# Kernel optimization log

Hardware: AMD Instinct MI355X
Metric: run time of the kernel (lower is better)

Reference implementation:

```python
import jax, jax.numpy as jnp
import numpy as np

B, T, IN = 256, 60, 520
GATE_IN = 8                      # 5 + 3, hard-coded in module
MOE_RAW = IN - GATE_IN           # 512
MOE_IN = MOE_RAW + GATE_IN * T   # 992
HID = MOE_RAW + (GATE_IN * T) // 2  # 752 (Python precedence: a + b*c//2)
OUT = 512
E = 8


def _uniform(key, shape, bound):
    return jax.random.uniform(key, shape, jnp.float32, -bound, bound)


def setup_inputs() -> dict:
    key = jax.random.key(0)
    ks = jax.random.split(key, 16)
    X = jax.random.normal(ks[0], (B, T, IN), jnp.float32)
    # GRU: 2 layers, hidden = E, gate order r,z,n (torch convention)
    gb = 1.0 / np.sqrt(E)
    Wih0 = _uniform(ks[1], (3 * E, GATE_IN), gb)
    Whh0 = _uniform(ks[2], (3 * E, E), gb)
    bih0 = _uniform(ks[3], (3 * E,), gb)
    bhh0 = _uniform(ks[4], (3 * E,), gb)
    Wih1 = _uniform(ks[5], (3 * E, E), gb)
    Whh1 = _uniform(ks[6], (3 * E, E), gb)
    bih1 = _uniform(ks[7], (3 * E,), gb)
    bhh1 = _uniform(ks[8], (3 * E,), gb)
    # Expert banks: glorot-style uniform as in init_params, zero biases
    def bank(k, i, o):
        wb = np.sqrt(6.0 / (i * o))
        return _uniform(k, (E, i, o), wb)
    w1 = bank(ks[9], MOE_IN, HID); b1 = jnp.zeros((E, HID), jnp.float32)
    w2 = bank(ks[10], HID, HID);   b2 = jnp.zeros((E, HID), jnp.float32)
    w3 = bank(ks[11], HID, OUT);   b3 = jnp.zeros((E, OUT), jnp.float32)
    return dict(X=X, Wih0=Wih0, Whh0=Whh0, bih0=bih0, bhh0=bhh0,
                Wih1=Wih1, Whh1=Whh1, bih1=bih1, bhh1=bhh1,
                w1=w1, b1=b1, w2=w2, b2=b2, w3=w3, b3=b3)


def _gru_layer(x, Wih, Whh, bih, bhh):
    # x: [B, T, in] -> outputs [B, T, H]
    H = Whh.shape[1]
    h0 = jnp.zeros((x.shape[0], H), x.dtype)

    def step(h, xt):
        gi = xt @ Wih.T + bih
        gh = h @ Whh.T + bhh
        ir, iz, i_n = jnp.split(gi, 3, axis=-1)
        hr, hz, h_n = jnp.split(gh, 3, axis=-1)
        r = jax.nn.sigmoid(ir + hr)
        z = jax.nn.sigmoid(iz + hz)
        n = jnp.tanh(i_n + r * h_n)
        h_new = (1.0 - z) * n + z * h
        return h_new, h_new

    _, ys = jax.lax.scan(step, h0, jnp.swapaxes(x, 0, 1))
    return jnp.swapaxes(ys, 0, 1)


def _blend_layer(x, coef, w, b):
    # per-sample weight synthesis + apply: same math as
    # sum(coef[...,None,None]*w[None],dim=1) then sum(x[...,None]*W,dim=1)+b
    Wb = jnp.einsum('be,eih->bih', coef, w)   # [B, in, out]
    bb = coef @ b                              # [B, out]
    return jnp.einsum('bi,bih->bh', x, Wb) + bb


def reference(X, Wih0, Whh0, bih0, bhh0, Wih1, Whh1, bih1, bhh1,
              w1, b1, w2, b2, w3, b3):
    Xg = X[:, :, MOE_RAW:]                                   # [B, T, 8]
    Xm = jnp.concatenate(
        [X[:, -1, :MOE_RAW], X[:, :, -GATE_IN:].reshape(X.shape[0], -1)], -1)
    # gating: 2-layer GRU, softmax on last step of layer 2
    h1 = _gru_layer(Xg, Wih0, Whh0, bih0, bhh0)
    h2 = _gru_layer(h1, Wih1, Whh1, bih1, bhh1)
    Omega = jax.nn.softmax(h2[:, -1, :], axis=-1)            # [B, E]
    # expert MLP with blended per-sample weights
    a = jax.nn.elu(_blend_layer(Xm, Omega, w1, b1))
    a = jax.nn.elu(_blend_layer(a, Omega, w2, b2))
    Y = _blend_layer(a, Omega, w3, b3)
    return Y
```

## Files before the change

kernel.cpp:

```cpp
#include <hip/hip_runtime.h>
#include <cstdint>
#include <cstddef>

typedef __attribute__((ext_vector_type(8))) short short8;
typedef __attribute__((ext_vector_type(8))) unsigned short ushort8;
typedef __attribute__((ext_vector_type(4))) float f32x4;

#define AS1Q const __attribute__((address_space(1)))
#define AS3Q __attribute__((address_space(3)))

constexpr int T_N = 60, IN_N = 520, MOE_RAW_N = 512, MOE_IN_N = 992;
constexpr int HID_N = 752, E_N = 8;
constexpr int K2_N = 6016;
constexpr int KA_N = 1024;
constexpr int SPLITK = 20;

static __device__ __forceinline__ unsigned short f2bf(float f) {
  unsigned int u = __float_as_uint(f);
  return (unsigned short)((u + 0x7fffu + ((u >> 16) & 1u)) >> 16);
}
static __device__ __forceinline__ float sigf(float x) {
  return __fdividef(1.f, 1.f + __expf(-x));
}
static __device__ __forceinline__ float tanh_fast(float x) {
  return 2.f * __fdividef(1.f, 1.f + __expf(-2.f * x)) - 1.f;
}

template<int R>
static __device__ __forceinline__ float rotf(float v) {
  return __int_as_float(__builtin_amdgcn_update_dpp(
      0, __float_as_int(v), 0x120 | R, 0xF, 0xF, true));
}
static __device__ __forceinline__ void rot8(float (&d)[8], float v) {
  d[0] = v;
  d[1] = rotf<1>(v); d[2] = rotf<2>(v); d[3] = rotf<3>(v);
  d[4] = rotf<4>(v); d[5] = rotf<5>(v); d[6] = rotf<6>(v); d[7] = rotf<7>(v);
}

__global__ __launch_bounds__(256)
void xm_prep(const float* __restrict__ X, unsigned short* __restrict__ XmBf)
{
  const int i = blockIdx.x * 256 + threadIdx.x;
  const int b = blockIdx.y;
  const float* Xb = X + (size_t)b * (T_N * IN_N);
  float v = 0.f;
  if (i < MOE_RAW_N) {
    v = Xb[(T_N - 1) * IN_N + i];
  } else if (i < MOE_IN_N) {
    const int q = i - MOE_RAW_N;
    v = Xb[(q >> 3) * IN_N + MOE_RAW_N + (q & 7)];
  }
  XmBf[(size_t)b * KA_N + (i ^ ((b & 7) << 3))] = f2bf(v);
}

__global__ __launch_bounds__(256, 1)
void fused_gru_gemm1(const float* __restrict__ X,
                     const float* __restrict__ Wih0, const float* __restrict__ Whh0,
                     const float* __restrict__ bih0, const float* __restrict__ bhh0,
                     const float* __restrict__ Wih1, const float* __restrict__ Whh1,
                     const float* __restrict__ bih1, const float* __restrict__ bhh1,
                     const unsigned short* __restrict__ XmBf,
                     const float* __restrict__ w1,
                     float* __restrict__ Y1, float* __restrict__ Omega)
{
  __shared__ union SM {
    struct { unsigned short Al[2][256][64]; unsigned short Bl[2][64][64]; } g;
    float xl[T_N][256];
  } sm;

  const int tid  = threadIdx.x;
  const int lane = tid & 63;
  const int wave = tid >> 6;

  if (blockIdx.x < 16) {
    const int j = tid & 7;
    const int b = blockIdx.x * 16 + (tid >> 4);

    const float* xsrc = X + (size_t)b * (T_N * IN_N) + MOE_RAW_N + j;
#pragma unroll
    for (int t = 0; t < T_N; ++t) {
      __builtin_amdgcn_global_load_lds((AS1Q unsigned int*)(xsrc + t * IN_N),
                                       (AS3Q unsigned int*)&sm.xl[t][wave * 64], 4, 0, 0);
    }

    const int got = __builtin_amdgcn_update_dpp(0, j, 0x121, 0xF, 0xF, true);
    const bool plus = (got == ((j + 1) & 7));

    float wi0r[8], wi0z[8], wi0n[8], wh0r[8], wh0z[8], wh0n[8];
    float wi1r[8], wi1z[8], wi1n[8], wh1r[8], wh1z[8], wh1n[8];
#pragma unroll
    for (int r = 0; r < 8; ++r) {
      const int i = plus ? ((j + r) & 7) : ((j - r) & 7);
      wi0r[r] = Wih0[j * 8 + i]; wi0z[r] = Wih0[(8 + j) * 8 + i]; wi0n[r] = Wih0[(16 + j) * 8 + i];
      wh0r[r] = Whh0[j * 8 + i]; wh0z[r] = Whh0[(8 + j) * 8 + i]; wh0n[r] = Whh0[(16 + j) * 8 + i];
      wi1r[r] = Wih1[j * 8 + i]; wi1z[r] = Wih1[(8 + j) * 8 + i]; wi1n[r] = Wih1[(16 + j) * 8 + i];
      wh1r[r] = Whh1[j * 8 + i]; wh1z[r] = Whh1[(8 + j) * 8 + i]; wh1n[r] = Whh1[(16 + j) * 8 + i];
    }
    const float br0 = bih0[j] + bhh0[j], bz0 = bih0[8 + j] + bhh0[8 + j];
    const float bin0 = bih0[16 + j],     bhn0 = bhh0[16 + j];
    const float br1 = bih1[j] + bhh1[j], bz1 = bih1[8 + j] + bhh1[8 + j];
    const float bin1 = bih1[16 + j],     bhn1 = bhh1[16 + j];

    __syncthreads();

    float h1 = 0.f, h2 = 0.f;
    float xcur = sm.xl[0][tid];

#pragma unroll 1
    for (int t = 0; t <= T_N; ++t) {
      const float xnext = sm.xl[(t + 1 < T_N) ? t + 1 : T_N - 1][tid];

      float rx[8];  rot8(rx, xcur);
      float rh1[8]; rot8(rh1, h1);
      float rh2[8]; rot8(rh2, h2);

      float grA = br0, gzA = bz0, gnA = bin0, hnA = bhn0;
      float grB = 0.f, gzB = 0.f, gnB = 0.f, hnB = 0.f;
#pragma unroll
      for (int r = 0; r < 4; ++r) {
        grA += wi0r[r] * rx[r];     gzA += wi0z[r] * rx[r];     gnA += wi0n[r] * rx[r];
        grA += wh0r[r] * rh1[r];    gzA += wh0z[r] * rh1[r];    hnA += wh0n[r] * rh1[r];
        grB += wi0r[4+r] * rx[4+r]; gzB += wi0z[4+r] * rx[4+r]; gnB += wi0n[4+r] * rx[4+r];
        grB += wh0r[4+r] * rh1[4+r];gzB += wh0z[4+r] * rh1[4+r];hnB += wh0n[4+r] * rh1[4+r];
      }
      float h1n;
      {
        const float r0 = sigf(grA + grB), z0 = sigf(gzA + gzB);
        const float n0 = tanh_fast((gnA + gnB) + r0 * (hnA + hnB));
        h1n = (1.f - z0) * n0 + z0 * h1;
      }

      float grA1 = br1, gzA1 = bz1, gnA1 = bin1, hnA1 = bhn1;
      float grB1 = 0.f, gzB1 = 0.f, gnB1 = 0.f, hnB1 = 0.f;
#pragma unroll
      for (int r = 0; r < 4; ++r) {
        grA1 += wi1r[r] * rh1[r];     gzA1 += wi1z[r] * rh1[r];     gnA1 += wi1n[r] * rh1[r];
        grA1 += wh1r[r] * rh2[r];     gzA1 += wh1z[r] * rh2[r];     hnA1 += wh1n[r] * rh2[r];
        grB1 += wi1r[4+r] * rh1[4+r]; gzB1 += wi1z[4+r] * rh1[4+r]; gnB1 += wi1n[4+r] * rh1[4+r];
        grB1 += wh1r[4+r] * rh2[4+r]; gzB1 += wh1z[4+r] * rh2[4+r]; hnB1 += wh1n[4+r] * rh2[4+r];
      }
      float h2n;
      {
        const float r1 = sigf(grA1 + grB1), z1 = sigf(gzA1 + gzB1);
        const float n1 = tanh_fast((gnA1 + gnB1) + r1 * (hnA1 + hnB1));
        h2n = (1.f - z1) * n1 + z1 * h2;
      }

      h1 = h1n;
      h2 = (t == 0) ? 0.f : h2n;
      xcur = xnext;
    }

    float rv[8]; rot8(rv, h2);
    float m = rv[0];
#pragma unroll
    for (int r = 1; r < 8; ++r) m = fmaxf(m, rv[r]);
    const float ej = __expf(h2 - m);
    float re[8]; rot8(re, ej);
    float sden = 0.f;
#pragma unroll
    for (int r = 0; r < 8; ++r) sden += re[r];
    if (!(tid & 8)) Omega[b * 8 + j] = __fdividef(ej, sden);
    return;
  }

  const int bid = blockIdx.x - 16;
  const int sp  = bid / 96;
  const int rr0 = bid - sp * 96;
  const int e   = rr0 & 7;
  const int nt  = rr0 >> 3;
  const int n0  = nt * 64;
  const int kt0 = sp * 8, kt1 = kt0 + 8;

  const int r15 = lane & 15, hi4 = lane >> 4, r7 = lane & 7;

  const unsigned short* Abase = XmBf + (size_t)(wave * 64 + (lane >> 3)) * KA_N + (lane & 7) * 8;
  const int bn = lane;
  const int kq = wave;
  const bool nvalid = (n0 + bn) < HID_N;
  const float* Bbase = w1 + ((size_t)e * MOE_IN_N + kq * 16) * HID_N + (n0 + bn);

  f32x4 acc[4][4];
  const f32x4 zero4 = {0.f, 0.f, 0.f, 0.f};
#pragma unroll
  for (int mi = 0; mi < 4; ++mi)
#pragma unroll
    for (int ni = 0; ni < 4; ++ni) acc[mi][ni] = zero4;

  auto stage = [&](int bufi, int kt) {
    const unsigned short* ga = Abase + kt * 64;
#pragma unroll
    for (int it = 0; it < 8; ++it) {
      __builtin_amdgcn_global_load_lds(
          (AS1Q unsigned int*)(ga + (size_t)it * 8 * KA_N),
          (AS3Q unsigned int*)&sm.g.Al[bufi][wave * 64 + it * 8][0],
          16, 0, 0);
    }
    const int kbase = kt * 64 + kq * 16;
    const float* gb = Bbase + (size_t)kt * 64 * HID_N;
    float v[16];
#pragma unroll
    for (int jj = 0; jj < 16; ++jj)
      v[jj] = (nvalid && (kbase + jj) < MOE_IN_N) ? gb[(size_t)jj * HID_N] : 0.f;
    ushort8 p0, p1;
#pragma unroll
    for (int jj = 0; jj < 8; ++jj) { p0[jj] = f2bf(v[jj]); p1[jj] = f2bf(v[jj + 8]); }
    const int sl0 = ((kq * 2) ^ (bn & 7)) * 8;
    const int sl1 = ((kq * 2 + 1) ^ (bn & 7)) * 8;
    *(ushort8*)&sm.g.Bl[bufi][bn][sl0] = p0;
    *(ushort8*)&sm.g.Bl[bufi][bn][sl1] = p1;
  };

  auto compute = [&](int bufi) {
#pragma unroll
    for (int ki = 0; ki < 2; ++ki) {
      const int ch = ((ki * 4 + hi4) ^ r7) * 8;
      short8 af[4], bfv[4];
#pragma unroll
      for (int mi = 0; mi < 4; ++mi)
        af[mi] = *(const short8*)&sm.g.Al[bufi][wave * 64 + mi * 16 + r15][ch];
#pragma unroll
      for (int ni = 0; ni < 4; ++ni)
        bfv[ni] = *(const short8*)&sm.g.Bl[bufi][ni * 16 + r15][ch];
#pragma unroll
      for (int mi = 0; mi < 4; ++mi)
#pragma unroll
        for (int ni = 0; ni < 4; ++ni)
          acc[mi][ni] = __builtin_amdgcn_mfma_f32_16x16x32_bf16(af[mi], bfv[ni], acc[mi][ni], 0, 0, 0);
    }
  };

  stage(0, kt0);
  __syncthreads();
  int buf = 0;
  for (int kt = kt0; kt < kt1; ++kt) {
    if (kt + 1 < kt1) stage(buf ^ 1, kt + 1);
    compute(buf);
    __syncthreads();
    buf ^= 1;
  }

  float* Pp = Y1 + ((size_t)(sp * 8 + e) * 256) * 768 + n0;
#pragma unroll
  for (int mi = 0; mi < 4; ++mi) {
    const int row = wave * 64 + mi * 16 + hi4 * 4;
#pragma unroll
    for (int ni = 0; ni < 4; ++ni) {
#pragma unroll
      for (int rq = 0; rq < 4; ++rq)
        Pp[(size_t)(row + rq) * 768 + ni * 16 + r15] = acc[mi][ni][rq];
    }
  }
}

__global__ __launch_bounds__(256)
void reduce1_mix(const float* __restrict__ Y1, const float* __restrict__ Omega,
                 const float* __restrict__ bias, unsigned short* __restrict__ xnext)
{
  const int n = blockIdx.x * 256 + threadIdx.x;
  const int b = blockIdx.y;
  if (n >= HID_N) return;
  float om[8];
#pragma unroll
  for (int e = 0; e < 8; ++e) om[e] = Omega[b * 8 + e];
  float acc = 0.f, bs = 0.f;
#pragma unroll
  for (int e = 0; e < 8; ++e) {
    const float ye = Y1[((size_t)e * 256 + b) * 768 + n]
                   + Y1[((size_t)(8 + e) * 256 + b) * 768 + n];
    acc += om[e] * ye;
    bs  += om[e] * bias[(size_t)e * HID_N + n];
  }
  const float y = acc + bs;
  const float a = (y > 0.f) ? y : expm1f(y);
  const int swz = (b & 7) << 3;
  unsigned short* row = xnext + (size_t)b * K2_N;
#pragma unroll
  for (int e = 0; e < 8; ++e)
    row[(e * HID_N + n) ^ swz] = f2bf(om[e] * a);
}

__global__ __launch_bounds__(256)
void gemm_splitk(const unsigned short* __restrict__ A,
                 const float* __restrict__ Bw,
                 float* __restrict__ P,
                 int K, int N, int NPAD)
{
  __shared__ unsigned short Al[2][256][64];
  __shared__ unsigned short Bl[2][64][64];

  const int tid = threadIdx.x;
  const int lane = tid & 63;
  const int wave = tid >> 6;
  const int nt = blockIdx.x, sp = blockIdx.y;
  const int n0 = nt * 64;
  const int KT = K >> 6;
  const int kt0 = (KT * sp) / SPLITK;
  const int kt1 = (KT * (sp + 1)) / SPLITK;

  const int r15 = lane & 15, hi4 = lane >> 4, r7 = lane & 7;

  const unsigned short* Abase = A + (size_t)(wave * 64 + (lane >> 3)) * K + (lane & 7) * 8;
  const int bn = lane;
  const int kq = wave;
  const bool nvalid = (n0 + bn) < N;
  const float* Bbase = Bw + (size_t)(kq * 16) * N + (n0 + bn);

  f32x4 acc[4][4];
  const f32x4 zero4 = {0.f, 0.f, 0.f, 0.f};
#pragma unroll
  for (int mi = 0; mi < 4; ++mi)
#pragma unroll
    for (int ni = 0; ni < 4; ++ni) acc[mi][ni] = zero4;

  auto stage = [&](int bufi, int kt) {
    const unsigned short* ga = Abase + kt * 64;
#pragma unroll
    for (int it = 0; it < 8; ++it) {
      __builtin_amdgcn_global_load_lds(
          (AS1Q unsigned int*)(ga + (size_t)it * 8 * K),
          (AS3Q unsigned int*)&Al[bufi][wave * 64 + it * 8][0],
          16, 0, 0);
    }
    const float* gb = Bbase + (size_t)kt * 64 * N;
    float v[16];
#pragma unroll
    for (int jj = 0; jj < 16; ++jj) v[jj] = nvalid ? gb[(size_t)jj * N] : 0.f;
    ushort8 p0, p1;
#pragma unroll
    for (int jj = 0; jj < 8; ++jj) { p0[jj] = f2bf(v[jj]); p1[jj] = f2bf(v[jj + 8]); }
    const int sl0 = ((kq * 2) ^ (bn & 7)) * 8;
    const int sl1 = ((kq * 2 + 1) ^ (bn & 7)) * 8;
    *(ushort8*)&Bl[bufi][bn][sl0] = p0;
    *(ushort8*)&Bl[bufi][bn][sl1] = p1;
  };

  auto compute = [&](int bufi) {
#pragma unroll
    for (int ki = 0; ki < 2; ++ki) {
      const int ch = ((ki * 4 + hi4) ^ r7) * 8;
      short8 af[4], bfv[4];
#pragma unroll
      for (int mi = 0; mi < 4; ++mi)
        af[mi] = *(const short8*)&Al[bufi][wave * 64 + mi * 16 + r15][ch];
#pragma unroll
      for (int ni = 0; ni < 4; ++ni)
        bfv[ni] = *(const short8*)&Bl[bufi][ni * 16 + r15][ch];
#pragma unroll
      for (int mi = 0; mi < 4; ++mi)
#pragma unroll
        for (int ni = 0; ni < 4; ++ni)
          acc[mi][ni] = __builtin_amdgcn_mfma_f32_16x16x32_bf16(af[mi], bfv[ni], acc[mi][ni], 0, 0, 0);
    }
  };

  stage(0, kt0);
  __syncthreads();
  int buf = 0;
  for (int kt = kt0; kt < kt1; ++kt) {
    if (kt + 1 < kt1) stage(buf ^ 1, kt + 1);
    compute(buf);
    __syncthreads();
    buf ^= 1;
  }

  float* Pp = P + (size_t)sp * 256 * NPAD + n0;
#pragma unroll
  for (int mi = 0; mi < 4; ++mi) {
    const int row = wave * 64 + mi * 16 + hi4 * 4;
#pragma unroll
    for (int ni = 0; ni < 4; ++ni) {
#pragma unroll
      for (int rq = 0; rq < 4; ++rq)
        Pp[(size_t)(row + rq) * NPAD + ni * 16 + r15] = acc[mi][ni][rq];
    }
  }
}

__global__ __launch_bounds__(256)
void reduce_mix_kernel(const float* __restrict__ P, const float* __restrict__ Omega,
                       const float* __restrict__ bias, unsigned short* __restrict__ xnext,
                       float* __restrict__ Yout, int N, int NPAD)
{
  const int n = blockIdx.x * 256 + threadIdx.x;
  const int b = blockIdx.y;
  if (n >= N) return;
  float acc = 0.f;
#pragma unroll 4
  for (int s = 0; s < SPLITK; ++s) acc += P[((size_t)s * 256 + b) * NPAD + n];
  float om[8];
#pragma unroll
  for (int e = 0; e < 8; ++e) om[e] = Omega[b * 8 + e];
  float bs = 0.f;
#pragma unroll
  for (int e = 0; e < 8; ++e) bs += om[e] * bias[(size_t)e * N + n];
  float y = acc + bs;
  if (Yout) { Yout[(size_t)b * N + n] = y; return; }
  float a = (y > 0.f) ? y : expm1f(y);
  const int swz = (b & 7) << 3;
  unsigned short* row = xnext + (size_t)b * K2_N;
#pragma unroll
  for (int e = 0; e < 8; ++e)
    row[(e * HID_N + n) ^ swz] = f2bf(om[e] * a);
}

extern "C" void kernel_launch(void* const* d_in, const int* in_sizes, int n_in,
                              void* d_out, int out_size, void* d_ws, size_t ws_size,
                              hipStream_t stream) {
  const float* X    = (const float*)d_in[0];
  const float* Wih0 = (const float*)d_in[1];
  const float* Whh0 = (const float*)d_in[2];
  const float* bih0 = (const float*)d_in[3];
  const float* bhh0 = (const float*)d_in[4];
  const float* Wih1 = (const float*)d_in[5];
  const float* Whh1 = (const float*)d_in[6];
  const float* bih1 = (const float*)d_in[7];
  const float* bhh1 = (const float*)d_in[8];
  const float* w1   = (const float*)d_in[9];
  const float* b1   = (const float*)d_in[10];
  const float* w2   = (const float*)d_in[11];
  const float* b2   = (const float*)d_in[12];
  const float* w3   = (const float*)d_in[13];
  const float* b3   = (const float*)d_in[14];

  char* ws = (char*)d_ws;
  float* Omega         = (float*)ws;
  unsigned short* XmBf = (unsigned short*)(ws + 8192);
  unsigned short* xt2  = (unsigned short*)(ws + 532480);
  unsigned short* xt3  = (unsigned short*)(ws + 3612672);
  float* Y1            = (float*)(ws + 6692864);
  float* P             = (float*)(ws + 19275776);

  xm_prep<<<dim3(4, 256), 256, 0, stream>>>(X, XmBf);

  fused_gru_gemm1<<<208, 256, 0, stream>>>(X, Wih0, Whh0, bih0, bhh0,
                                           Wih1, Whh1, bih1, bhh1,
                                           XmBf, w1, Y1, Omega);

  reduce1_mix<<<dim3(3, 256), 256, 0, stream>>>(Y1, Omega, b1, xt2);

  gemm_splitk<<<dim3(12, SPLITK), 256, 0, stream>>>(xt2, w2, P, K2_N, HID_N, 768);
  reduce_mix_kernel<<<dim3(3, 256), 256, 0, stream>>>(P, Omega, b2, xt3, nullptr, HID_N, 768);

  gemm_splitk<<<dim3(8, SPLITK), 256, 0, stream>>>(xt3, w3, P, K2_N, 512, 512);
  reduce_mix_kernel<<<dim3(2, 256), 256, 0, stream>>>(P, Omega, b3, nullptr, (float*)d_out, 512, 512);
}
```

Before: 84.47 us.

## Fuse Xm gather into GEMM1, drop its split-K, and use atomic split-K reduction

Removes the xm_prep kernel: GEMM1 now gathers and converts the X slices to bf16 directly into shared memory, and runs the full K range in 96 blocks instead of two K halves. The later split-K GEMMs accumulate into a single P buffer with float atomics, replacing the 20-way partial buffer and its reduction pass. Consumers zero P for the next stage. The intent is fewer launches and less partial-sum traffic. In exchange, GEMM1 has half as many blocks, each with twice the K loop. Atomic contention and non-deterministic summation order are added.

```diff
diff --git a/kernel.cpp b/kernel.cpp
--- a/kernel.cpp
+++ b/kernel.cpp
@@ -14,6 +14,7 @@
 constexpr int K2_N = 6016;
 constexpr int KA_N = 1024;
 constexpr int SPLITK = 20;
+constexpr int PN = 768;
 
 static __device__ __forceinline__ unsigned short f2bf(float f) {
   unsigned int u = __float_as_uint(f);
@@ -35,22 +36,6 @@
   d[0] = v;
   d[1] = rotf<1>(v); d[2] = rotf<2>(v); d[3] = rotf<3>(v);
   d[4] = rotf<4>(v); d[5] = rotf<5>(v); d[6] = rotf<6>(v); d[7] = rotf<7>(v);
-}
-
-__global__ __launch_bounds__(256)
-void xm_prep(const float* __restrict__ X, unsigned short* __restrict__ XmBf)
-{
-  const int i = blockIdx.x * 256 + threadIdx.x;
-  const int b = blockIdx.y;
-  const float* Xb = X + (size_t)b * (T_N * IN_N);
-  float v = 0.f;
-  if (i < MOE_RAW_N) {
-    v = Xb[(T_N - 1) * IN_N + i];
-  } else if (i < MOE_IN_N) {
-    const int q = i - MOE_RAW_N;
-    v = Xb[(q >> 3) * IN_N + MOE_RAW_N + (q & 7)];
-  }
-  XmBf[(size_t)b * KA_N + (i ^ ((b & 7) << 3))] = f2bf(v);
 }
 
 __global__ __launch_bounds__(256, 1)
@@ -59,7 +44,6 @@
                      const float* __restrict__ bih0, const float* __restrict__ bhh0,
                      const float* __restrict__ Wih1, const float* __restrict__ Whh1,
                      const float* __restrict__ bih1, const float* __restrict__ bhh1,
-                     const unsigned short* __restrict__ XmBf,
                      const float* __restrict__ w1,
                      float* __restrict__ Y1, float* __restrict__ Omega)
 {
@@ -165,16 +149,14 @@
   }
 
   const int bid = blockIdx.x - 16;
-  const int sp  = bid / 96;
-  const int rr0 = bid - sp * 96;
-  const int e   = rr0 & 7;
-  const int nt  = rr0 >> 3;
+  const int e   = bid & 7;
+  const int nt  = bid >> 3;
   const int n0  = nt * 64;
-  const int kt0 = sp * 8, kt1 = kt0 + 8;
 
   const int r15 = lane & 15, hi4 = lane >> 4, r7 = lane & 7;
-
-  const unsigned short* Abase = XmBf + (size_t)(wave * 64 + (lane >> 3)) * KA_N + (lane & 7) * 8;
+  const int g = lane >> 3, c = lane & 7;
+  const int sw = ((c ^ g) << 3);
+
   const int bn = lane;
   const int kq = wave;
   const bool nvalid = (n0 + bn) < HID_N;
@@ -188,13 +170,23 @@
     for (int ni = 0; ni < 4; ++ni) acc[mi][ni] = zero4;
 
   auto stage = [&](int bufi, int kt) {
-    const unsigned short* ga = Abase + kt * 64;
+    const int k0 = kt * 64 + c * 8;
 #pragma unroll
     for (int it = 0; it < 8; ++it) {
-      __builtin_amdgcn_global_load_lds(
-          (AS1Q unsigned int*)(ga + (size_t)it * 8 * KA_N),
-          (AS3Q unsigned int*)&sm.g.Al[bufi][wave * 64 + it * 8][0],
-          16, 0, 0);
+      const int row = wave * 64 + g + it * 8;
+      f32x4 v0 = zero4, v1 = zero4;
+      if (k0 < MOE_RAW_N) {
+        const float* p = X + (size_t)row * (T_N * IN_N) + (T_N - 1) * IN_N + k0;
+        v0 = *(const f32x4*)p; v1 = *(const f32x4*)(p + 4);
+      } else if (k0 < MOE_IN_N) {
+        const int tt = (k0 - MOE_RAW_N) >> 3;
+        const float* p = X + (size_t)row * (T_N * IN_N) + tt * IN_N + MOE_RAW_N;
+        v0 = *(const f32x4*)p; v1 = *(const f32x4*)(p + 4);
+      }
+      ushort8 pk;
+#pragma unroll
+      for (int jj = 0; jj < 4; ++jj) { pk[jj] = f2bf(v0[jj]); pk[4 + jj] = f2bf(v1[jj]); }
+      *(ushort8*)&sm.g.Al[bufi][row][sw] = pk;
     }
     const int kbase = kt * 64 + kq * 16;
     const float* gb = Bbase + (size_t)kt * 64 * HID_N;
@@ -222,6 +214,130 @@
 #pragma unroll
       for (int ni = 0; ni < 4; ++ni)
         bfv[ni] = *(const short8*)&sm.g.Bl[bufi][ni * 16 + r15][ch];
+#pragma unroll
+      for (int mi = 0; mi < 4; ++mi)
+#pragma unroll
+        for (int ni = 0; ni < 4; ++ni)
+          acc[mi][ni] = __builtin_amdgcn_mfma_f32_16x16x32_bf16(af[mi], bfv[ni], acc[mi][ni], 0, 0, 0);
+    }
+  };
+
+  stage(0, 0);
+  __syncthreads();
+  int buf = 0;
+  for (int kt = 0; kt < 16; ++kt) {
+    if (kt + 1 < 16) stage(buf ^ 1, kt + 1);
+    compute(buf);
+    __syncthreads();
+    buf ^= 1;
+  }
+
+  float* Pp = Y1 + ((size_t)e * 256) * PN + n0;
+#pragma unroll
+  for (int mi = 0; mi < 4; ++mi) {
+    const int row = wave * 64 + mi * 16 + hi4 * 4;
+#pragma unroll
+    for (int ni = 0; ni < 4; ++ni) {
+#pragma unroll
+      for (int rq = 0; rq < 4; ++rq)
+        Pp[(size_t)(row + rq) * PN + ni * 16 + r15] = acc[mi][ni][rq];
+    }
+  }
+}
+
+__global__ __launch_bounds__(256)
+void reduce1_mix(const float* __restrict__ Y1, const float* __restrict__ Omega,
+                 const float* __restrict__ bias, unsigned short* __restrict__ xnext,
+                 float* __restrict__ P)
+{
+  const int n = blockIdx.x * 256 + threadIdx.x;
+  const int b = blockIdx.y;
+  P[(size_t)b * PN + n] = 0.f;
+  if (n >= HID_N) return;
+  float om[8];
+#pragma unroll
+  for (int e = 0; e < 8; ++e) om[e] = Omega[b * 8 + e];
+  float acc = 0.f, bs = 0.f;
+#pragma unroll
+  for (int e = 0; e < 8; ++e) {
+    acc += om[e] * Y1[((size_t)e * 256 + b) * PN + n];
+    bs  += om[e] * bias[(size_t)e * HID_N + n];
+  }
+  const float y = acc + bs;
+  const float a = (y > 0.f) ? y : expm1f(y);
+  const int swz = (b & 7) << 3;
+  unsigned short* row = xnext + (size_t)b * K2_N;
+#pragma unroll
+  for (int e = 0; e < 8; ++e)
+    row[(e * HID_N + n) ^ swz] = f2bf(om[e] * a);
+}
+
+__global__ __launch_bounds__(256)
+void gemm_splitk_atomic(const unsigned short* __restrict__ A,
+                        const float* __restrict__ Bw,
+                        float* __restrict__ P,
+                        int K, int N)
+{
+  __shared__ unsigned short Al[2][256][64];
+  __shared__ unsigned short Bl[2][64][64];
+
+  const int tid = threadIdx.x;
+  const int lane = tid & 63;
+  const int wave = tid >> 6;
+  const int nt = blockIdx.x, sp = blockIdx.y;
+  const int n0 = nt * 64;
+  const int KT = K >> 6;
+  const int kt0 = (KT * sp) / SPLITK;
+  const int kt1 = (KT * (sp + 1)) / SPLITK;
+
+  const int r15 = lane & 15, hi4 = lane >> 4, r7 = lane & 7;
+
+  const unsigned short* Abase = A + (size_t)(wave * 64 + (lane >> 3)) * K + (lane & 7) * 8;
+  const int bn = lane;
+  const int kq = wave;
+  const bool nvalid = (n0 + bn) < N;
+  const float* Bbase = Bw + (size_t)(kq * 16) * N + (n0 + bn);
+
+  f32x4 acc[4][4];
+  const f32x4 zero4 = {0.f, 0.f, 0.f, 0.f};
+#pragma unroll
+  for (int mi = 0; mi < 4; ++mi)
+#pragma unroll
+    for (int ni = 0; ni < 4; ++ni) acc[mi][ni] = zero4;
+
+  auto stage = [&](int bufi, int kt) {
+    const unsigned short* ga = Abase + kt * 64;
+#pragma unroll
+    for (int it = 0; it < 8; ++it) {
+      __builtin_amdgcn_global_load_lds(
+          (AS1Q unsigned int*)(ga + (size_t)it * 8 * K),
+          (AS3Q unsigned int*)&Al[bufi][wave * 64 + it * 8][0],
+          16, 0, 0);
+    }
+    const float* gb = Bbase + (size_t)kt * 64 * N;
+    float v[16];
+#pragma unroll
+    for (int jj = 0; jj < 16; ++jj) v[jj] = nvalid ? gb[(size_t)jj * N] : 0.f;
+    ushort8 p0, p1;
+#pragma unroll
+    for (int jj = 0; jj < 8; ++jj) { p0[jj] = f2bf(v[jj]); p1[jj] = f2bf(v[jj + 8]); }
+    const int sl0 = ((kq * 2) ^ (bn & 7)) * 8;
+    const int sl1 = ((kq * 2 + 1) ^ (bn & 7)) * 8;
+    *(ushort8*)&Bl[bufi][bn][sl0] = p0;
+    *(ushort8*)&Bl[bufi][bn][sl1] = p1;
+  };
+
+  auto compute = [&](int bufi) {
+#pragma unroll
+    for (int ki = 0; ki < 2; ++ki) {
+      const int ch = ((ki * 4 + hi4) ^ r7) * 8;
+      short8 af[4], bfv[4];
+#pragma unroll
+      for (int mi = 0; mi < 4; ++mi)
+        af[mi] = *(const short8*)&Al[bufi][wave * 64 + mi * 16 + r15][ch];
+#pragma unroll
+      for (int ni = 0; ni < 4; ++ni)
+        bfv[ni] = *(const short8*)&Bl[bufi][ni * 16 + r15][ch];
 #pragma unroll
       for (int mi = 0; mi < 4; ++mi)
 #pragma unroll
@@ -240,7 +356,7 @@
     buf ^= 1;
   }
 
-  float* Pp = Y1 + ((size_t)(sp * 8 + e) * 256) * 768 + n0;
+  float* Pp = P + n0;
 #pragma unroll
   for (int mi = 0; mi < 4; ++mi) {
     const int row = wave * 64 + mi * 16 + hi4 * 4;
@@ -248,155 +364,33 @@
     for (int ni = 0; ni < 4; ++ni) {
 #pragma unroll
       for (int rq = 0; rq < 4; ++rq)
-        Pp[(size_t)(row + rq) * 768 + ni * 16 + r15] = acc[mi][ni][rq];
+        atomicAdd(&Pp[(size_t)(row + rq) * PN + ni * 16 + r15], acc[mi][ni][rq]);
     }
   }
 }
 
 __global__ __launch_bounds__(256)
-void reduce1_mix(const float* __restrict__ Y1, const float* __restrict__ Omega,
-                 const float* __restrict__ bias, unsigned short* __restrict__ xnext)
+void reduce_p(float* __restrict__ P, const float* __restrict__ Omega,
+              const float* __restrict__ bias, unsigned short* __restrict__ xnext,
+              float* __restrict__ Yout, int N, int zeroP)
 {
   const int n = blockIdx.x * 256 + threadIdx.x;
   const int b = blockIdx.y;
-  if (n >= HID_N) return;
-  float om[8];
-#pragma unroll
-  for (int e = 0; e < 8; ++e) om[e] = Omega[b * 8 + e];
-  float acc = 0.f, bs = 0.f;
-#pragma unroll
-  for (int e = 0; e < 8; ++e) {
-    const float ye = Y1[((size_t)e * 256 + b) * 768 + n]
-                   + Y1[((size_t)(8 + e) * 256 + b) * 768 + n];
-    acc += om[e] * ye;
-    bs  += om[e] * bias[(size_t)e * HID_N + n];
-  }
-  const float y = acc + bs;
-  const float a = (y > 0.f) ? y : expm1f(y);
-  const int swz = (b & 7) << 3;
-  unsigned short* row = xnext + (size_t)b * K2_N;
-#pragma unroll
-  for (int e = 0; e < 8; ++e)
-    row[(e * HID_N + n) ^ swz] = f2bf(om[e] * a);
-}
-
-__global__ __launch_bounds__(256)
-void gemm_splitk(const unsigned short* __restrict__ A,
-                 const float* __restrict__ Bw,
-                 float* __restrict__ P,
-                 int K, int N, int NPAD)
-{
-  __shared__ unsigned short Al[2][256][64];
-  __shared__ unsigned short Bl[2][64][64];
-
-  const int tid = threadIdx.x;
-  const int lane = tid & 63;
-  const int wave = tid >> 6;
-  const int nt = blockIdx.x, sp = blockIdx.y;
-  const int n0 = nt * 64;
-  const int KT = K >> 6;
-  const int kt0 = (KT * sp) / SPLITK;
-  const int kt1 = (KT * (sp + 1)) / SPLITK;
-
-  const int r15 = lane & 15, hi4 = lane >> 4, r7 = lane & 7;
-
-  const unsigned short* Abase = A + (size_t)(wave * 64 + (lane >> 3)) * K + (lane & 7) * 8;
-  const int bn = lane;
-  const int kq = wave;
-  const bool nvalid = (n0 + bn) < N;
-  const float* Bbase = Bw + (size_t)(kq * 16) * N + (n0 + bn);
-
-  f32x4 acc[4][4];
-  const f32x4 zero4 = {0.f, 0.f, 0.f, 0.f};
-#pragma unroll
-  for (int mi = 0; mi < 4; ++mi)
-#pragma unroll
-    for (int ni = 0; ni < 4; ++ni) acc[mi][ni] = zero4;
-
-  auto stage = [&](int bufi, int kt) {
-    const unsigned short* ga = Abase + kt * 64;
-#pragma unroll
-    for (int it = 0; it < 8; ++it) {
-      __builtin_amdgcn_global_load_lds(
-          (AS1Q unsigned int*)(ga + (size_t)it * 8 * K),
-          (AS3Q unsigned int*)&Al[bufi][wave * 64 + it * 8][0],
-          16, 0, 0);
-    }
-    const float* gb = Bbase + (size_t)kt * 64 * N;
-    float v[16];
-#pragma unroll
-    for (int jj = 0; jj < 16; ++jj) v[jj] = nvalid ? gb[(size_t)jj * N] : 0.f;
-    ushort8 p0, p1;
-#pragma unroll
-    for (int jj = 0; jj < 8; ++jj) { p0[jj] = f2bf(v[jj]); p1[jj] = f2bf(v[jj + 8]); }
-    const int sl0 = ((kq * 2) ^ (bn & 7)) * 8;
-    const int sl1 = ((kq * 2 + 1) ^ (bn & 7)) * 8;
-    *(ushort8*)&Bl[bufi][bn][sl0] = p0;
-    *(ushort8*)&Bl[bufi][bn][sl1] = p1;
-  };
-
-  auto compute = [&](int bufi) {
-#pragma unroll
-    for (int ki = 0; ki < 2; ++ki) {
-      const int ch = ((ki * 4 + hi4) ^ r7) * 8;
-      short8 af[4], bfv[4];
-#pragma unroll
-      for (int mi = 0; mi < 4; ++mi)
-        af[mi] = *(const short8*)&Al[bufi][wave * 64 + mi * 16 + r15][ch];
-#pragma unroll
-      for (int ni = 0; ni < 4; ++ni)
-        bfv[ni] = *(const short8*)&Bl[bufi][ni * 16 + r15][ch];
-#pragma unroll
-      for (int mi = 0; mi < 4; ++mi)
-#pragma unroll
-        for (int ni = 0; ni < 4; ++ni)
-          acc[mi][ni] = __builtin_amdgcn_mfma_f32_16x16x32_bf16(af[mi], bfv[ni], acc[mi][ni], 0, 0, 0);
-    }
-  };
-
-  stage(0, kt0);
-  __syncthreads();
-  int buf = 0;
-  for (int kt = kt0; kt < kt1; ++kt) {
-    if (kt + 1 < kt1) stage(buf ^ 1, kt + 1);
-    compute(buf);
-    __syncthreads();
-    buf ^= 1;
-  }
-
-  float* Pp = P + (size_t)sp * 256 * NPAD + n0;
-#pragma unroll
-  for (int mi = 0; mi < 4; ++mi) {
-    const int row = wave * 64 + mi * 16 + hi4 * 4;
-#pragma unroll
-    for (int ni = 0; ni < 4; ++ni) {
-#pragma unroll
-      for (int rq = 0; rq < 4; ++rq)
-        Pp[(size_t)(row + rq) * NPAD + ni * 16 + r15] = acc[mi][ni][rq];
-    }
-  }
-}
-
-__global__ __launch_bounds__(256)
-void reduce_mix_kernel(const float* __restrict__ P, const float* __restrict__ Omega,
-                       const float* __restrict__ bias, unsigned short* __restrict__ xnext,
-                       float* __restrict__ Yout, int N, int NPAD)
-{
-  const int n = blockIdx.x * 256 + threadIdx.x;
-  const int b = blockIdx.y;
+  float v = 0.f;
+  if (n < PN) {
+    v = P[(size_t)b * PN + n];
+    if (zeroP) P[(size_t)b * PN + n] = 0.f;
+  }
   if (n >= N) return;
-  float acc = 0.f;
-#pragma unroll 4
-  for (int s = 0; s < SPLITK; ++s) acc += P[((size_t)s * 256 + b) * NPAD + n];
   float om[8];
 #pragma unroll
   for (int e = 0; e < 8; ++e) om[e] = Omega[b * 8 + e];
   float bs = 0.f;
 #pragma unroll
   for (int e = 0; e < 8; ++e) bs += om[e] * bias[(size_t)e * N + n];
-  float y = acc + bs;
+  const float y = v + bs;
   if (Yout) { Yout[(size_t)b * N + n] = y; return; }
-  float a = (y > 0.f) ? y : expm1f(y);
+  const float a = (y > 0.f) ? y : expm1f(y);
   const int swz = (b & 7) << 3;
   unsigned short* row = xnext + (size_t)b * K2_N;
 #pragma unroll
@@ -424,24 +418,21 @@
   const float* b3   = (const float*)d_in[14];
 
   char* ws = (char*)d_ws;
-  float* Omega         = (float*)ws;
-  unsigned short* XmBf = (unsigned short*)(ws + 8192);
-  unsigned short* xt2  = (unsigned short*)(ws + 532480);
-  unsigned short* xt3  = (unsigned short*)(ws + 3612672);
-  float* Y1            = (float*)(ws + 6692864);
-  float* P             = (float*)(ws + 19275776);
-
-  xm_prep<<<dim3(4, 256), 256, 0, stream>>>(X, XmBf);
-
-  fused_gru_gemm1<<<208, 256, 0, stream>>>(X, Wih0, Whh0, bih0, bhh0,
+  float* Omega        = (float*)ws;
+  unsigned short* xt2 = (unsigned short*)(ws + 8192);
+  unsigned short* xt3 = (unsigned short*)(ws + 3088384);
+  float* Y1           = (float*)(ws + 6168576);
+  float* P            = (float*)(ws + 12460032);
+
+  fused_gru_gemm1<<<112, 256, 0, stream>>>(X, Wih0, Whh0, bih0, bhh0,
                                            Wih1, Whh1, bih1, bhh1,
-                                           XmBf, w1, Y1, Omega);
-
-  reduce1_mix<<<dim3(3, 256), 256, 0, stream>>>(Y1, Omega, b1, xt2);
-
-  gemm_splitk<<<dim3(12, SPLITK), 256, 0, stream>>>(xt2, w2, P, K2_N, HID_N, 768);
-  reduce_mix_kernel<<<dim3(3, 256), 256, 0, stream>>>(P, Omega, b2, xt3, nullptr, HID_N, 768);
-
-  gemm_splitk<<<dim3(8, SPLITK), 256, 0, stream>>>(xt3, w3, P, K2_N, 512, 512);
-  reduce_mix_kernel<<<dim3(2, 256), 256, 0, stream>>>(P, Omega, b3, nullptr, (float*)d_out, 512, 512);
-}
+                                           w1, Y1, Omega);
+
+  reduce1_mix<<<dim3(3, 256), 256, 0, stream>>>(Y1, Omega, b1, xt2, P);
+
+  gemm_splitk_atomic<<<dim3(12, SPLITK), 256, 0, stream>>>(xt2, w2, P, K2_N, HID_N);
+  reduce_p<<<dim3(3, 256), 256, 0, stream>>>(P, Omega, b2, xt3, nullptr, HID_N, 1);
+
+  gemm_splitk_atomic<<<dim3(8, SPLITK), 256, 0, stream>>>(xt3, w3, P, K2_N, 512);
+  reduce_p<<<dim3(2, 256), 256, 0, stream>>>(P, Omega, b3, nullptr, (float*)d_out, 512, 0);
+}
```

Measured after the change: 133.8 us. +58.4%, slower.
